# Optimization experiments

Hardware: AMD Instinct MI355X
Metric: run time of the kernel (lower is better)

## Reference

```python
import jax, jax.numpy as jnp
import numpy as np

B, N, E = 128, 100, 800          # graphs, nodes/graph, edges/graph
TN, TE = B * N, B * E
NODE_EMB, REL_EMB, H = 128, 256, 256   # hidden_size == relation_emb in CoMPILE
R, DEPTH = 200, 3
EDGE_EMB = 2 * NODE_EMB + REL_EMB      # 512


def _gru_dir(x, h0, w_ih, w_hh, b_ih, b_hh):
    """One direction of a torch-style GRU. x: [B,T,H], h0: [B,H] -> [B,T,H]."""
    def step(h, xt):
        gi = xt @ w_ih.T + b_ih
        gh = h @ w_hh.T + b_hh
        i_r, i_z, i_n = jnp.split(gi, 3, axis=-1)
        h_r, h_z, h_n = jnp.split(gh, 3, axis=-1)
        r = jax.nn.sigmoid(i_r + h_r)
        z = jax.nn.sigmoid(i_z + h_z)
        n = jnp.tanh(i_n + r * h_n)
        hn = (1.0 - z) * n + z * h
        return hn, hn
    _, ys = jax.lax.scan(step, h0, jnp.swapaxes(x, 0, 1))
    return jnp.swapaxes(ys, 0, 1)


def setup_inputs() -> dict:
    key = jax.random.key(0)
    ks = iter(jax.random.split(key, 40))
    def w(shape):
        return jax.random.normal(next(ks), shape, jnp.float32) * 0.05
    inp = {}
    inp["node_feat"] = jax.random.normal(next(ks), (TN, NODE_EMB), jnp.float32)
    inp["rel_emb"] = jax.random.normal(next(ks), (R, REL_EMB), jnp.float32)  # final_relation_embeddings
    # model weights (bias=False everywhere except W_o, linear1, gru)
    inp["W_i_node"] = w((H, NODE_EMB))
    inp["W_i_edge"] = w((H, EDGE_EMB))
    inp["Wa1"] = w((H, 2 * H))          # input_attention1
    inp["Wa2"] = w((1, H))              # input_attention2
    inp["W_h_atom"] = w((DEPTH - 1, H, H))
    inp["W_h_bond"] = w((DEPTH - 1, H, H))
    inp["Wd1"] = w((DEPTH - 1, H, H + REL_EMB))  # Attention1_d
    inp["Wd2"] = w((DEPTH - 1, 1, H))            # Attention2_d
    inp["W_comm"] = w((H, 3 * H))       # communicate_mlp
    inp["gru_bias"] = w((H,))
    inp["w_ih_f"] = w((3 * H, H)); inp["w_hh_f"] = w((3 * H, H))
    inp["b_ih_f"] = w((3 * H,));   inp["b_hh_f"] = w((3 * H,))
    inp["w_ih_b"] = w((3 * H, H)); inp["w_hh_b"] = w((3 * H, H))
    inp["b_ih_b"] = w((3 * H,));   inp["b_hh_b"] = w((3 * H,))
    inp["W_o"] = w((H, 2 * H)); inp["b_o"] = w((H,))
    inp["W_lin1"] = w((1, H)); inp["b_lin1"] = w((1,))
    # graph structure: edges stay inside their own subgraph (block-diagonal batching)
    off = (jnp.arange(B, dtype=jnp.int64)[:, None] * N)
    inp["edge_src"] = (jax.random.randint(next(ks), (B, E), 0, N) + off).reshape(-1)
    inp["edge_dst"] = (jax.random.randint(next(ks), (B, E), 0, N) + off).reshape(-1)
    inp["edge_rel"] = jax.random.randint(next(ks), (TE,), 0, R)
    inp["batch_rel"] = jax.random.randint(next(ks), (B,), 0, R)
    inp["src_node"] = jax.random.randint(next(ks), (B,), 0, N) + jnp.arange(B) * N
    inp["tgt_node"] = jax.random.randint(next(ks), (B,), 0, N) + jnp.arange(B) * N
    return inp


def reference(node_feat, rel_emb, W_i_node, W_i_edge, Wa1, Wa2, W_h_atom, W_h_bond,
              Wd1, Wd2, W_comm, gru_bias, w_ih_f, w_hh_f, b_ih_f, b_hh_f,
              w_ih_b, w_hh_b, b_ih_b, b_hh_b, W_o, b_o, W_lin1, b_lin1,
              edge_src, edge_dst, edge_rel, batch_rel, src_node, tgt_node):
    act = jax.nn.relu  # args.activation = 'ReLU'
    tgt_rel = rel_emb[batch_rel]                              # [B,H] per-query relation
    e_rel = rel_emb[edge_rel]                                 # [TE,H]
    edge_feat = jnp.concatenate([node_feat[edge_src], e_rel, node_feat[edge_dst]], 1)  # [TE,EDGE_EMB]
    input_node = act(node_feat @ W_i_node.T)                  # [TN,H]
    message_node = input_node
    input_edge = act(edge_feat @ W_i_edge.T)                  # [TE,H]
    message_edge = input_edge
    edge_tgt_rel = jnp.repeat(tgt_rel, E, axis=0)             # [TE,H] target relation per edge
    total_source = jnp.repeat(src_node, E)                    # [TE] query head node per edge
    total_target = jnp.repeat(tgt_node, E)
    # input edge attention vs translational query embedding
    g_edge = message_node[total_source] + edge_tgt_rel - message_node[total_target]
    att = jnp.tanh(jnp.concatenate([message_edge, g_edge], 1) @ Wa1.T)
    att = jax.nn.sigmoid(att @ Wa2.T)
    message_edge = message_edge * att
    for d in range(DEPTH - 1):
        # edge->node aggregation (MySpMM with target-side incidence e2n_sp)
        agg = jax.ops.segment_sum(message_edge, edge_dst, num_segments=TN)
        message_node = act((message_node + agg) @ W_h_atom[d].T)
        # node->edge (e2n_sp2^T: gather source-node states per edge)
        message_edge = act(input_edge + message_node[edge_src] @ W_h_bond[d].T)
        att = jnp.tanh(jnp.concatenate([message_edge, edge_tgt_rel], 1) @ Wd1[d].T)
        att = jax.nn.sigmoid(att @ Wd2[d].T)
        message_edge = message_edge * att
    agg = jax.ops.segment_sum(message_edge, edge_dst, num_segments=TN)
    agg2 = jnp.concatenate([agg, message_node, input_node], 1) @ W_comm.T  # [TN,H]
    # BatchGRU: uniform graph sizes -> pad/unpad is a reshape
    msg = act(agg2 + gru_bias).reshape(B, N, H)
    h0 = agg2.reshape(B, N, H).max(axis=1)                    # per-graph max of hidden
    out_f = _gru_dir(msg, h0, w_ih_f, w_hh_f, b_ih_f, b_hh_f)
    out_b = _gru_dir(msg[:, ::-1], h0, w_ih_b, w_hh_b, b_ih_b, b_hh_b)[:, ::-1]
    a_message = act(jnp.concatenate([out_f, out_b], -1).reshape(TN, 2 * H))
    atom_h = act(a_message @ W_o.T + b_o)                     # [TN,H]
    conv = jnp.tanh(atom_h[src_node] + tgt_rel - atom_h[tgt_node])  # [B,H]
    return conv @ W_lin1.T + b_lin1                           # [B,1]
```

## Files before the change

kernel.cpp:

```cpp
#include <hip/hip_runtime.h>
#include <cstddef>

#define Bg 128
#define Nn 100
#define Eg 800
#define TNODE 12800
#define TEDGE 102400
#define HD 256
#define NEMB 128
#define REMB 256

typedef short bf8 __attribute__((ext_vector_type(8)));
typedef short bf4 __attribute__((ext_vector_type(4)));
typedef float f4  __attribute__((ext_vector_type(4)));

__device__ __forceinline__ float relu_(float x){ return x > 0.f ? x : 0.f; }
__device__ __forceinline__ float sigm_(float x){ return 1.f/(1.f + __expf(-x)); }
__device__ __forceinline__ float4 ld4(const float* p){ return *(const float4*)p; }
__device__ __forceinline__ void st4(float* p, float4 v){ *(float4*)p = v; }
__device__ __forceinline__ float4 add4(float4 a, float4 b){
    return float4{a.x+b.x, a.y+b.y, a.z+b.z, a.w+b.w};
}
__device__ __forceinline__ float4 relu4(float4 a){
    return float4{relu_(a.x), relu_(a.y), relu_(a.z), relu_(a.w)};
}
__device__ __forceinline__ short f2bf(float f){
    unsigned u = __float_as_uint(f);
    u += 0x7fff + ((u >> 16) & 1);
    return (short)(u >> 16);
}
__device__ __forceinline__ float bf2f(short s){
    return __uint_as_float(((unsigned)(unsigned short)s) << 16);
}
__device__ __forceinline__ void split4(float4 v, bf4& h, bf4& l){
    h.x = f2bf(v.x); l.x = f2bf(v.x - bf2f(h.x));
    h.y = f2bf(v.y); l.y = f2bf(v.y - bf2f(h.y));
    h.z = f2bf(v.z); l.z = f2bf(v.z - bf2f(h.z));
    h.w = f2bf(v.w); l.w = f2bf(v.w - bf2f(h.w));
}
__device__ __forceinline__ f4 mfma_(bf8 a, bf8 b, f4 c){
    return __builtin_amdgcn_mfma_f32_16x16x32_bf16(a, b, c, 0, 0, 0);
}

enum { A_PLAIN=0, A_ADD=1, A_RELUB=2, A_CLAMP=3, A_CAT3=4, A_CAT2R=5 };
enum { E_STORE=0, E_RELU=1, E_BIAS=2, E_BIASRELU=3 };

template<int AM, int EM>
__global__ __launch_bounds__(256, 2)
void mgemm(const float* __restrict__ A0, const float* __restrict__ A1,
           const float* __restrict__ A2, const float* __restrict__ W,
           const float* __restrict__ bias, float* __restrict__ C,
           int M, int N, int K, int lda, int wld)
{
    __shared__ short Ah[128][40], Al[128][40], Bh[128][40], Bl[128][40];
    const int t  = threadIdx.x;
    const int kc = t & 7, lr = t >> 3;
    const int lane = t & 63, wv = t >> 6;
    const int wm = wv >> 1, wn = wv & 1;
    const int frow = lane & 15, fk = (lane >> 4) * 8;
    const int row0 = blockIdx.y * 128, col0 = blockIdx.x * 128;

    f4 acc[4][4] = {};

    for (int k0 = 0; k0 < K; k0 += 32) {
        const int gk = k0 + kc * 4;
        const int kk = kc * 4;
        #pragma unroll
        for (int ri = 0; ri < 4; ri++) {
            int row = lr + 32 * ri;
            int grow = row0 + row;
            float4 v;
            if (AM == A_PLAIN) {
                v = ld4(A0 + (size_t)grow * lda + gk);
            } else if (AM == A_ADD) {
                v = add4(ld4(A0 + (size_t)grow * lda + gk),
                         ld4(A1 + (size_t)grow * lda + gk));
            } else if (AM == A_RELUB) {
                v = relu4(add4(ld4(A0 + (size_t)grow * lda + gk), ld4(A1 + gk)));
            } else if (AM == A_CLAMP) {
                int cr = grow < M ? grow : M - 1;
                v = ld4(A0 + (size_t)cr * lda + gk);
            } else if (AM == A_CAT3) {
                if (gk < HD)        v = ld4(A0 + (size_t)grow * HD + gk);
                else if (gk < 2*HD) v = ld4(A1 + (size_t)grow * HD + gk - HD);
                else                v = ld4(A2 + (size_t)grow * HD + gk - 2*HD);
            } else {
                v = (gk < HD) ? relu4(ld4(A0 + (size_t)grow * HD + gk))
                              : relu4(ld4(A1 + (size_t)grow * HD + gk - HD));
            }
            bf4 h, l; split4(v, h, l);
            *(bf4*)&Ah[row][kk] = h;
            *(bf4*)&Al[row][kk] = l;
        }
        #pragma unroll
        for (int ri = 0; ri < 4; ri++) {
            int wr = lr + 32 * ri;
            float4 v = ld4(W + (size_t)(col0 + wr) * wld + gk);
            bf4 h, l; split4(v, h, l);
            *(bf4*)&Bh[wr][kk] = h;
            *(bf4*)&Bl[wr][kk] = l;
        }
        __syncthreads();
        bf8 ah[4], al[4], bh[4], bl[4];
        #pragma unroll
        for (int mi = 0; mi < 4; mi++) {
            ah[mi] = *(const bf8*)&Ah[wm*64 + mi*16 + frow][fk];
            al[mi] = *(const bf8*)&Al[wm*64 + mi*16 + frow][fk];
        }
        #pragma unroll
        for (int ni = 0; ni < 4; ni++) {
            bh[ni] = *(const bf8*)&Bh[wn*64 + ni*16 + frow][fk];
            bl[ni] = *(const bf8*)&Bl[wn*64 + ni*16 + frow][fk];
        }
        #pragma unroll
        for (int mi = 0; mi < 4; mi++)
            #pragma unroll
            for (int ni = 0; ni < 4; ni++) {
                acc[mi][ni] = mfma_(ah[mi], bh[ni], acc[mi][ni]);
                acc[mi][ni] = mfma_(ah[mi], bl[ni], acc[mi][ni]);
                acc[mi][ni] = mfma_(al[mi], bh[ni], acc[mi][ni]);
            }
        __syncthreads();
    }
    #pragma unroll
    for (int mi = 0; mi < 4; mi++) {
        #pragma unroll
        for (int ni = 0; ni < 4; ni++) {
            int ccol = col0 + wn*64 + ni*16 + frow;
            int rbase = row0 + wm*64 + mi*16 + (lane >> 4) * 4;
            #pragma unroll
            for (int reg = 0; reg < 4; reg++) {
                float v = acc[mi][ni][reg];
                if (EM == E_BIAS || EM == E_BIASRELU) v += bias[ccol];
                if (EM == E_RELU || EM == E_BIASRELU) v = relu_(v);
                C[(size_t)(rbase + reg) * N + ccol] = v;
            }
        }
    }
}

__global__ void w1split_kernel(const float* __restrict__ Wa1, const float* __restrict__ Wd1,
                               short* __restrict__ w1h, short* __restrict__ w1l)
{
    int idx = blockIdx.x * 256 + threadIdx.x;
    int which = idx >> 16, rem = idx & 65535;
    int r = rem >> 8, k = rem & 255;
    const float* W = (which == 0) ? Wa1 : (Wd1 + (size_t)(which - 1) * 256 * 512);
    float v = W[(size_t)r * 512 + k];
    short hi = f2bf(v);
    w1h[idx] = hi;
    w1l[idx] = f2bf(v - bf2f(hi));
}

template<int MODE>
__global__ __launch_bounds__(256, 2)
void mattn(const float* __restrict__ S, const float* __restrict__ Rt,
           const float* __restrict__ D, const float* __restrict__ T0,
           const int* __restrict__ esrc, const int* __restrict__ erel,
           const int* __restrict__ edst,
           const short* __restrict__ w1h, const short* __restrict__ w1l,
           const float* __restrict__ W2,
           const float* __restrict__ term, float* __restrict__ sbuf)
{
    __shared__ short Ah[128][40], Al[128][40];
    __shared__ float partl[4][128];
    __shared__ int isrc[128], irel[128], idst[128];
    const int t = threadIdx.x;
    const int kc = t & 7, lr = t >> 3;
    const int lane = t & 63, wv = t >> 6;
    const int frow = lane & 15, kb = (lane >> 4) * 8;
    const int r0 = blockIdx.x * 128;

    if (t < 128) {
        int e = r0 + t;
        isrc[t] = esrc[e]; irel[t] = erel[e]; idst[t] = edst[e];
    }
    __syncthreads();

    f4 acc[8][4] = {};

    for (int k0 = 0; k0 < 8; k0++) {
        const int gk = k0 * 32 + kc * 4;
        const int kk = kc * 4;
        #pragma unroll
        for (int ri = 0; ri < 4; ri++) {
            int row = lr + 32 * ri;
            int s = isrc[row], rl = irel[row], dd = idst[row];
            float4 v = relu4(add4(add4(ld4(S + (size_t)s * HD + gk),
                                       ld4(Rt + (size_t)rl * HD + gk)),
                                  ld4(D + (size_t)dd * HD + gk)));
            if (MODE) v = relu4(add4(v, ld4(T0 + (size_t)s * HD + gk)));
            bf4 h, l; split4(v, h, l);
            *(bf4*)&Ah[row][kk] = h;
            *(bf4*)&Al[row][kk] = l;
        }
        __syncthreads();
        bf8 ah[8], al[8];
        #pragma unroll
        for (int mi = 0; mi < 8; mi++) {
            ah[mi] = *(const bf8*)&Ah[mi*16 + frow][kb];
            al[mi] = *(const bf8*)&Al[mi*16 + frow][kb];
        }
        #pragma unroll
        for (int ni = 0; ni < 4; ni++) {
            int wr = wv*64 + ni*16 + frow;
            const short* wp = (const short*)w1h + (size_t)wr * 256 + k0*32 + kb;
            const short* lp = (const short*)w1l + (size_t)wr * 256 + k0*32 + kb;
            bf8 bh = *(const bf8*)wp;
            bf8 bl = *(const bf8*)lp;
            #pragma unroll
            for (int mi = 0; mi < 8; mi++) {
                acc[mi][ni] = mfma_(ah[mi], bh, acc[mi][ni]);
                acc[mi][ni] = mfma_(ah[mi], bl, acc[mi][ni]);
                acc[mi][ni] = mfma_(al[mi], bh, acc[mi][ni]);
            }
        }
        __syncthreads();
    }
    #pragma unroll
    for (int mi = 0; mi < 8; mi++) {
        #pragma unroll
        for (int reg = 0; reg < 4; reg++) {
            int rl = mi*16 + (lane >> 4) * 4 + reg;
            int g = (r0 + rl) / Eg;
            float p = 0.f;
            #pragma unroll
            for (int ni = 0; ni < 4; ni++) {
                int n = wv*64 + ni*16 + frow;
                p += tanhf(acc[mi][ni][reg] + term[g*HD + n]) * W2[n];
            }
            p += __shfl_xor(p, 1); p += __shfl_xor(p, 2);
            p += __shfl_xor(p, 4); p += __shfl_xor(p, 8);
            if (frow == 0) partl[wv][rl] = p;
        }
    }
    __syncthreads();
    if (t < 128) {
        float p = partl[0][t] + partl[1][t] + partl[2][t] + partl[3][t];
        sbuf[r0 + t] = sigm_(p);
    }
}

template<int MODE>
__global__ __launch_bounds__(256)
void agg_gather(const float* __restrict__ S, const float* __restrict__ Rt,
                const float* __restrict__ D, const float* __restrict__ T0,
                const int* __restrict__ esrc, const int* __restrict__ erel,
                const int* __restrict__ rowptr, const int* __restrict__ eidx,
                const float* __restrict__ s, float* __restrict__ agg)
{
    int node = blockIdx.x * 4 + (threadIdx.x >> 6);
    int c = (threadIdx.x & 63) * 4;
    float4 dn = ld4(D + (size_t)node * HD + c);
    float4 acc{0.f, 0.f, 0.f, 0.f};
    int beg = rowptr[node], end = rowptr[node + 1];
    for (int i = beg; i < end; i++) {
        int e = eidx[i];
        int sr = esrc[e], rl = erel[e];
        float4 v = relu4(add4(add4(ld4(S + (size_t)sr * HD + c),
                                   ld4(Rt + (size_t)rl * HD + c)), dn));
        if (MODE) v = relu4(add4(v, ld4(T0 + (size_t)sr * HD + c)));
        float sc = s[e];
        acc.x += v.x * sc; acc.y += v.y * sc;
        acc.z += v.z * sc; acc.w += v.w * sc;
    }
    st4(agg + (size_t)node * HD + c, acc);
}

__global__ void zeroi_kernel(int* __restrict__ p)
{
    p[blockIdx.x * 256 + threadIdx.x] = 0;
}
__global__ void csr_count(const int* __restrict__ dst, int* __restrict__ cnt)
{
    int e = blockIdx.x * 256 + threadIdx.x;
    atomicAdd(&cnt[dst[e]], 1);
}
__global__ void csr_scan(const int* __restrict__ cnt, int* __restrict__ rowptr)
{
    __shared__ int ws[4];
    __shared__ int carry;
    int tid = threadIdx.x;
    if (tid == 0) carry = 0;
    __syncthreads();
    for (int i = 0; i < TNODE; i += 256) {
        int v = cnt[i + tid];
        int x = v;
        #pragma unroll
        for (int off = 1; off < 64; off <<= 1) {
            int y = __shfl_up(x, off);
            if ((tid & 63) >= off) x += y;
        }
        if ((tid & 63) == 63) ws[tid >> 6] = x;
        __syncthreads();
        int add = carry;
        int w = tid >> 6;
        for (int j = 0; j < w; j++) add += ws[j];
        rowptr[i + tid] = add + x - v;
        __syncthreads();
        if (tid == 255) carry = add + x;
        __syncthreads();
    }
    if (tid == 0) rowptr[TNODE] = carry;
}
__global__ void csr_fill(const int* __restrict__ dst, const int* __restrict__ rowptr,
                         int* __restrict__ fillc, int* __restrict__ eidx)
{
    int e = blockIdx.x * 256 + threadIdx.x;
    int d = dst[e];
    int slot = rowptr[d] + atomicAdd(&fillc[d], 1);
    eidx[slot] = e;
}

__global__ __launch_bounds__(256)
void term_kernel(const float* __restrict__ mn, const float* __restrict__ tgt_rel,
                 const float* __restrict__ Wa1, const float* __restrict__ Wd1,
                 const int* __restrict__ srcn, const int* __restrict__ tgtn,
                 float* __restrict__ term)
{
    __shared__ float Gs[HD];
    int b = blockIdx.x % Bg;
    int which = blockIdx.x / Bg;
    int c = threadIdx.x;
    float g;
    if (which == 0)
        g = mn[(size_t)srcn[b]*HD + c] + tgt_rel[b*HD + c] - mn[(size_t)tgtn[b]*HD + c];
    else
        g = tgt_rel[b*HD + c];
    Gs[c] = g;
    __syncthreads();
    const float* W = (which == 0) ? Wa1 : (Wd1 + (size_t)(which-1)*HD*512);
    float p = 0.f;
    for (int k = 0; k < HD; k += 4) {
        float4 w = ld4(W + (size_t)c*512 + 256 + k);
        p = fmaf(Gs[k], w.x, p); p = fmaf(Gs[k+1], w.y, p);
        p = fmaf(Gs[k+2], w.z, p); p = fmaf(Gs[k+3], w.w, p);
    }
    term[(size_t)which*Bg*HD + b*HD + c] = p;
}

__global__ void tgtrel_kernel(const float* __restrict__ rel_emb, const int* __restrict__ batch_rel,
                              float* __restrict__ tgt_rel)
{
    int b = blockIdx.x, c = threadIdx.x;
    tgt_rel[b*HD + c] = rel_emb[(size_t)batch_rel[b]*REMB + c];
}

__global__ void h0_kernel(const float* __restrict__ agg2, float* __restrict__ h0)
{
    int b = blockIdx.x, c = threadIdx.x;
    float m = -1e30f;
    for (int n = 0; n < Nn; n++)
        m = fmaxf(m, agg2[((size_t)b*Nn + n)*HD + c]);
    h0[b*HD + c] = m;
}

__global__ void whbf_kernel(const float* __restrict__ whf, const float* __restrict__ whb,
                            short* __restrict__ whbf)
{
    int idx = blockIdx.x * 256 + threadIdx.x;
    int d = idx / (768*256), rem = idx % (768*256);
    whbf[idx] = f2bf((d ? whb : whf)[rem]);
}

__global__ void biascomb_kernel(const float* __restrict__ bihf, const float* __restrict__ bhhf,
                                const float* __restrict__ bihb, const float* __restrict__ bhhb,
                                float* __restrict__ bc)
{
    int i = blockIdx.x * 256 + threadIdx.x;
    int d = i / 768, r = i % 768;
    const float* bi = d ? bihb : bihf;
    const float* bhh = d ? bhhb : bhhf;
    bc[i] = bi[r] + (r < 512 ? bhh[r] : 0.f);
}

__global__ __launch_bounds__(512, 2)
void gru_seq(const float* __restrict__ gi_f, const float* __restrict__ gi_b,
             const short* __restrict__ whbf,
             const float* __restrict__ bhf, const float* __restrict__ bhb,
             const float* __restrict__ h0,
             float* __restrict__ outf, float* __restrict__ outb)
{
    __shared__ float hsf[16][260];
    __shared__ short hsh[16][264];
    __shared__ short hsl[16][264];
    __shared__ float gates[768][17];
    const int blk = blockIdx.x;
    const int d = blk >> 3, grp = blk & 7;
    const int tid = threadIdx.x;
    const int lane = tid & 63, wv = tid >> 6;
    const int f16 = lane & 15;
    const int kb  = (lane >> 4) * 8;

    const short* wp0 = whbf + (size_t)d * 768 * 256;
    const float* gi  = d ? gi_b : gi_f;
    const float* bh  = d ? bhb : bhf;
    float* outp      = d ? outb : outf;

    const int eseq = tid >> 5, ehb = tid & 31;
    float bhn[8];
    #pragma unroll
    for (int hh = 0; hh < 8; hh++) bhn[hh] = bh[512 + ehb + hh * 32];

    {
        #pragma unroll
        for (int hh = 0; hh < 8; hh++) {
            int h = ehb + hh * 32;
            float v = h0[(size_t)(grp*16 + eseq) * HD + h];
            hsf[eseq][h] = v;
            short hi = f2bf(v);
            hsh[eseq][h] = hi;
            hsl[eseq][h] = f2bf(v - bf2f(hi));
        }
    }
    __syncthreads();

    for (int t = 0; t < Nn; t++) {
        int trow = d ? (Nn - 1 - t) : t;
        float gr[8], gz[8], gn[8];
        {
            size_t girow = ((size_t)(grp*16 + eseq) * Nn + trow) * 768;
            #pragma unroll
            for (int hh = 0; hh < 8; hh++) {
                int h = ehb + hh * 32;
                gr[hh] = gi[girow + h];
                gz[hh] = gi[girow + 256 + h];
                gn[hh] = gi[girow + 512 + h];
            }
        }
        #pragma unroll
        for (int j = 0; j < 6; j++) {
            int wr = (wv*6 + j) * 16 + f16;
            const short* wp = wp0 + (size_t)wr * 256 + kb;
            f4 acc = {};
            #pragma unroll
            for (int ks = 0; ks < 8; ks++) {
                bf8 ahi = *(const bf8*)&hsh[f16][ks*32 + kb];
                bf8 alo = *(const bf8*)&hsl[f16][ks*32 + kb];
                bf8 b = *(const bf8*)(wp + ks*32);
                acc = mfma_(ahi, b, acc);
                acc = mfma_(alo, b, acc);
            }
            #pragma unroll
            for (int reg = 0; reg < 4; reg++)
                gates[(wv*6 + j)*16 + f16][(lane >> 4)*4 + reg] = acc[reg];
        }
        __syncthreads();
        {
            size_t orow = ((size_t)(grp*16 + eseq) * Nn + trow) * HD;
            #pragma unroll
            for (int hh = 0; hh < 8; hh++) {
                int h = ehb + hh * 32;
                float R  = gates[h][eseq];
                float Z  = gates[256 + h][eseq];
                float NN = gates[512 + h][eseq];
                float hprev = hsf[eseq][h];
                float r = sigm_(gr[hh] + R);
                float z = sigm_(gz[hh] + Z);
                float n = tanhf(gn[hh] + r * (NN + bhn[hh]));
                float nh = (1.f - z) * n + z * hprev;
                hsf[eseq][h] = nh;
                short hi = f2bf(nh);
                hsh[eseq][h] = hi;
                hsl[eseq][h] = f2bf(nh - bf2f(hi));
                outp[orow + h] = nh;
            }
        }
        __syncthreads();
    }
}

__global__ __launch_bounds__(256)
void final_kernel(const float* __restrict__ atom_h, const float* __restrict__ tgt_rel,
                  const int* __restrict__ srcn, const int* __restrict__ tgtn,
                  const float* __restrict__ Wl, const float* __restrict__ bl,
                  float* __restrict__ out)
{
    __shared__ float red[4];
    int b = blockIdx.x, c = threadIdx.x;
    float v = tanhf(atom_h[(size_t)srcn[b]*HD + c] + tgt_rel[b*HD + c]
                    - atom_h[(size_t)tgtn[b]*HD + c]);
    float p = v * Wl[c];
    #pragma unroll
    for (int off = 1; off < 64; off <<= 1) p += __shfl_xor(p, off);
    int wv = c >> 6;
    if ((c & 63) == 0) red[wv] = p;
    __syncthreads();
    if (c == 0) out[b] = red[0] + red[1] + red[2] + red[3] + bl[0];
}

extern "C" void kernel_launch(void* const* d_in, const int* in_sizes, int n_in,
                              void* d_out, int out_size, void* d_ws, size_t ws_size,
                              hipStream_t stream)
{
    const float* node_feat = (const float*)d_in[0];
    const float* rel_emb   = (const float*)d_in[1];
    const float* W_i_node  = (const float*)d_in[2];
    const float* W_i_edge  = (const float*)d_in[3];
    const float* Wa1       = (const float*)d_in[4];
    const float* Wa2       = (const float*)d_in[5];
    const float* W_h_atom  = (const float*)d_in[6];
    const float* W_h_bond  = (const float*)d_in[7];
    const float* Wd1       = (const float*)d_in[8];
    const float* Wd2       = (const float*)d_in[9];
    const float* W_comm    = (const float*)d_in[10];
    const float* gru_bias  = (const float*)d_in[11];
    const float* w_ih_f    = (const float*)d_in[12];
    const float* w_hh_f    = (const float*)d_in[13];
    const float* b_ih_f    = (const float*)d_in[14];
    const float* b_hh_f    = (const float*)d_in[15];
    const float* w_ih_b    = (const float*)d_in[16];
    const float* w_hh_b    = (const float*)d_in[17];
    const float* b_ih_b    = (const float*)d_in[18];
    const float* b_hh_b    = (const float*)d_in[19];
    const float* W_o       = (const float*)d_in[20];
    const float* b_o       = (const float*)d_in[21];
    const float* W_lin1    = (const float*)d_in[22];
    const float* b_lin1    = (const float*)d_in[23];
    const int* edge_src  = (const int*)d_in[24];
    const int* edge_dst  = (const int*)d_in[25];
    const int* edge_rel  = (const int*)d_in[26];
    const int* batch_rel = (const int*)d_in[27];
    const int* src_node  = (const int*)d_in[28];
    const int* tgt_node  = (const int*)d_in[29];
    float* out = (float*)d_out;

    float* ws = (float*)d_ws;
    size_t off = 0;
    auto alloc = [&](size_t n){ float* p = ws + off; off += n; return p; };
    float* tgt_rel    = alloc((size_t)Bg*HD);
    float* term       = alloc((size_t)3*Bg*HD);
    float* input_node = alloc((size_t)TNODE*HD);
    float* mn_a       = alloc((size_t)TNODE*HD);
    float* mn_b       = alloc((size_t)TNODE*HD);
    float* agg        = alloc((size_t)TNODE*HD);
    float* h0v        = alloc((size_t)Bg*HD);
    short* whbf       = (short*)alloc((size_t)2*768*256/2);
    short* w1h        = (short*)alloc((size_t)3*256*256/2);
    short* w1l        = (short*)alloc((size_t)3*256*256/2);
    float* bcomb      = alloc((size_t)2*768);
    float* sbuf       = alloc((size_t)TEDGE);
    int*   cnt        = (int*)alloc((size_t)TNODE);
    int*   fillc      = (int*)alloc((size_t)TNODE);
    int*   rowptr     = (int*)alloc((size_t)TNODE + 256);
    int*   eidx       = (int*)alloc((size_t)TEDGE);
    float* Sbuf       = alloc((size_t)TNODE*HD);
    float* Dbuf       = alloc((size_t)TNODE*HD);
    float* Rbuf       = alloc((size_t)256*HD);
    float* gi_f       = alloc((size_t)TNODE*768);
    float* gi_b       = alloc((size_t)TNODE*768);
    float* out_f      = alloc((size_t)TNODE*HD);
    float* out_b      = alloc((size_t)TNODE*HD);
    float* agg2   = mn_a;
    float* atom_h = input_node;

    tgtrel_kernel<<<Bg, 256, 0, stream>>>(rel_emb, batch_rel, tgt_rel);
    whbf_kernel<<<1536, 256, 0, stream>>>(w_hh_f, w_hh_b, whbf);
    w1split_kernel<<<768, 256, 0, stream>>>(Wa1, Wd1, w1h, w1l);
    biascomb_kernel<<<6, 256, 0, stream>>>(b_ih_f, b_hh_f, b_ih_b, b_hh_b, bcomb);

    zeroi_kernel<<<2*TNODE/256, 256, 0, stream>>>(cnt);
    csr_count<<<TEDGE/256, 256, 0, stream>>>(edge_dst, cnt);
    csr_scan<<<1, 256, 0, stream>>>(cnt, rowptr);
    csr_fill<<<TEDGE/256, 256, 0, stream>>>(edge_dst, rowptr, fillc, eidx);

    mgemm<A_PLAIN, E_RELU><<<dim3(HD/128, TNODE/128), 256, 0, stream>>>(
        node_feat, nullptr, nullptr, W_i_node, nullptr, input_node,
        TNODE, HD, NEMB, NEMB, NEMB);

    mgemm<A_PLAIN, E_STORE><<<dim3(HD/128, TNODE/128), 256, 0, stream>>>(
        node_feat, nullptr, nullptr, W_i_edge + 0, nullptr, Sbuf,
        TNODE, HD, NEMB, NEMB, 512);
    mgemm<A_PLAIN, E_STORE><<<dim3(HD/128, TNODE/128), 256, 0, stream>>>(
        node_feat, nullptr, nullptr, W_i_edge + 384, nullptr, Dbuf,
        TNODE, HD, NEMB, NEMB, 512);
    mgemm<A_CLAMP, E_STORE><<<dim3(HD/128, 2), 256, 0, stream>>>(
        rel_emb, nullptr, nullptr, W_i_edge + 128, nullptr, Rbuf,
        200, HD, REMB, REMB, 512);

    term_kernel<<<3*Bg, 256, 0, stream>>>(input_node, tgt_rel, Wa1, Wd1,
                                          src_node, tgt_node, term);

    mattn<0><<<TEDGE/128, 256, 0, stream>>>(Sbuf, Rbuf, Dbuf, Sbuf,
        edge_src, edge_rel, edge_dst, w1h, w1l, Wa2, term, sbuf);
    agg_gather<0><<<TNODE/4, 256, 0, stream>>>(Sbuf, Rbuf, Dbuf, Sbuf,
        edge_src, edge_rel, rowptr, eidx, sbuf, agg);

    const float* mn_cur = input_node;
    float* bufs[2] = {mn_a, mn_b};
    for (int d = 0; d < 2; d++) {
        float* mn_next = bufs[d];
        float* tmp     = bufs[1-d];
        mgemm<A_ADD, E_RELU><<<dim3(2, TNODE/128), 256, 0, stream>>>(
            mn_cur, agg, nullptr, W_h_atom + (size_t)d*HD*HD, nullptr, mn_next,
            TNODE, HD, HD, HD, HD);
        mgemm<A_PLAIN, E_STORE><<<dim3(2, TNODE/128), 256, 0, stream>>>(
            mn_next, nullptr, nullptr, W_h_bond + (size_t)d*HD*HD, nullptr, tmp,
            TNODE, HD, HD, HD, HD);
        mattn<1><<<TEDGE/128, 256, 0, stream>>>(Sbuf, Rbuf, Dbuf, tmp,
            edge_src, edge_rel, edge_dst, w1h + (size_t)(1+d)*65536,
            w1l + (size_t)(1+d)*65536, Wd2 + (size_t)d*HD,
            term + (size_t)(1+d)*Bg*HD, sbuf);
        agg_gather<1><<<TNODE/4, 256, 0, stream>>>(Sbuf, Rbuf, Dbuf, tmp,
            edge_src, edge_rel, rowptr, eidx, sbuf, agg);
        mn_cur = mn_next;
    }

    mgemm<A_CAT3, E_STORE><<<dim3(2, TNODE/128), 256, 0, stream>>>(
        agg, (const float*)mn_cur, input_node, W_comm, nullptr, agg2,
        TNODE, HD, 3*HD, 0, 3*HD);

    h0_kernel<<<Bg, 256, 0, stream>>>(agg2, h0v);

    mgemm<A_RELUB, E_BIAS><<<dim3(768/128, TNODE/128), 256, 0, stream>>>(
        agg2, gru_bias, nullptr, w_ih_f, bcomb, gi_f,
        TNODE, 768, HD, HD, HD);
    mgemm<A_RELUB, E_BIAS><<<dim3(768/128, TNODE/128), 256, 0, stream>>>(
        agg2, gru_bias, nullptr, w_ih_b, bcomb + 768, gi_b,
        TNODE, 768, HD, HD, HD);

    gru_seq<<<16, 512, 0, stream>>>(gi_f, gi_b, whbf, b_hh_f, b_hh_b, h0v,
                                    out_f, out_b);

    mgemm<A_CAT2R, E_BIASRELU><<<dim3(2, TNODE/128), 256, 0, stream>>>(
        out_f, out_b, nullptr, W_o, b_o, atom_h,
        TNODE, HD, 2*HD, 0, 2*HD);

    final_kernel<<<Bg, 256, 0, stream>>>(atom_h, tgt_rel, src_node, tgt_node,
                                         W_lin1, b_lin1, out);
}
```

Before: 1.319 ms.

## Pre-split GEMM weights into bf16 hi/lo once, read B fragments from global

Adds a generic wsplit kernel that converts each weight matrix into bf16 high/low halves once per call. The GEMM kernel then loads B fragments straight from global memory instead of staging and splitting weights in shared memory every tile. It also halves LDS use and raises launch bounds to three blocks per CU. The intent is to remove repeated per-block weight conversion and the LDS traffic for B. In exchange it adds twelve small split launches and uncoalesced global loads for B fragments, which depend on L2 hits.

```diff
diff --git a/kernel.cpp b/kernel.cpp
--- a/kernel.cpp
+++ b/kernel.cpp
@@ -45,14 +45,27 @@
 enum { A_PLAIN=0, A_ADD=1, A_RELUB=2, A_CLAMP=3, A_CAT3=4, A_CAT2R=5 };
 enum { E_STORE=0, E_RELU=1, E_BIAS=2, E_BIASRELU=3 };
 
+__global__ void wsplit(const float* __restrict__ src, int ld, int K,
+                       short* __restrict__ h, short* __restrict__ l, int total)
+{
+    int idx = blockIdx.x * 256 + threadIdx.x;
+    if (idx >= total) return;
+    int r = idx / K, k = idx % K;
+    float v = src[(size_t)r * ld + k];
+    short hi = f2bf(v);
+    h[idx] = hi;
+    l[idx] = f2bf(v - bf2f(hi));
+}
+
 template<int AM, int EM>
-__global__ __launch_bounds__(256, 2)
-void mgemm(const float* __restrict__ A0, const float* __restrict__ A1,
-           const float* __restrict__ A2, const float* __restrict__ W,
+__global__ __launch_bounds__(256, 3)
+void mgemw(const float* __restrict__ A0, const float* __restrict__ A1,
+           const float* __restrict__ A2,
+           const short* __restrict__ Wh, const short* __restrict__ Wl,
            const float* __restrict__ bias, float* __restrict__ C,
-           int M, int N, int K, int lda, int wld)
-{
-    __shared__ short Ah[128][40], Al[128][40], Bh[128][40], Bl[128][40];
+           int M, int N, int K, int lda)
+{
+    __shared__ short Ah[128][40], Al[128][40];
     const int t  = threadIdx.x;
     const int kc = t & 7, lr = t >> 3;
     const int lane = t & 63, wv = t >> 6;
@@ -92,14 +105,6 @@
             *(bf4*)&Ah[row][kk] = h;
             *(bf4*)&Al[row][kk] = l;
         }
-        #pragma unroll
-        for (int ri = 0; ri < 4; ri++) {
-            int wr = lr + 32 * ri;
-            float4 v = ld4(W + (size_t)(col0 + wr) * wld + gk);
-            bf4 h, l; split4(v, h, l);
-            *(bf4*)&Bh[wr][kk] = h;
-            *(bf4*)&Bl[wr][kk] = l;
-        }
         __syncthreads();
         bf8 ah[4], al[4], bh[4], bl[4];
         #pragma unroll
@@ -109,8 +114,9 @@
         }
         #pragma unroll
         for (int ni = 0; ni < 4; ni++) {
-            bh[ni] = *(const bf8*)&Bh[wn*64 + ni*16 + frow][fk];
-            bl[ni] = *(const bf8*)&Bl[wn*64 + ni*16 + frow][fk];
+            int wr = col0 + wn*64 + ni*16 + frow;
+            bh[ni] = *(const bf8*)&Wh[(size_t)wr * K + k0 + fk];
+            bl[ni] = *(const bf8*)&Wl[(size_t)wr * K + k0 + fk];
         }
         #pragma unroll
         for (int mi = 0; mi < 4; mi++)
@@ -137,19 +143,6 @@
             }
         }
     }
-}
-
-__global__ void w1split_kernel(const float* __restrict__ Wa1, const float* __restrict__ Wd1,
-                               short* __restrict__ w1h, short* __restrict__ w1l)
-{
-    int idx = blockIdx.x * 256 + threadIdx.x;
-    int which = idx >> 16, rem = idx & 65535;
-    int r = rem >> 8, k = rem & 255;
-    const float* W = (which == 0) ? Wa1 : (Wd1 + (size_t)(which - 1) * 256 * 512);
-    float v = W[(size_t)r * 512 + k];
-    short hi = f2bf(v);
-    w1h[idx] = hi;
-    w1l[idx] = f2bf(v - bf2f(hi));
 }
 
 template<int MODE>
@@ -204,10 +197,8 @@
         #pragma unroll
         for (int ni = 0; ni < 4; ni++) {
             int wr = wv*64 + ni*16 + frow;
-            const short* wp = (const short*)w1h + (size_t)wr * 256 + k0*32 + kb;
-            const short* lp = (const short*)w1l + (size_t)wr * 256 + k0*32 + kb;
-            bf8 bh = *(const bf8*)wp;
-            bf8 bl = *(const bf8*)lp;
+            bf8 bh = *(const bf8*)(w1h + (size_t)wr * 256 + k0*32 + kb);
+            bf8 bl = *(const bf8*)(w1l + (size_t)wr * 256 + k0*32 + kb);
             #pragma unroll
             for (int mi = 0; mi < 8; mi++) {
                 acc[mi][ni] = mfma_(ah[mi], bh, acc[mi][ni]);
@@ -528,6 +519,7 @@
     float* ws = (float*)d_ws;
     size_t off = 0;
     auto alloc = [&](size_t n){ float* p = ws + off; off += n; return p; };
+    auto salloc = [&](size_t n){ short* p = (short*)(ws + off); off += (n + 1) / 2; return p; };
     float* tgt_rel    = alloc((size_t)Bg*HD);
     float* term       = alloc((size_t)3*Bg*HD);
     float* input_node = alloc((size_t)TNODE*HD);
@@ -535,9 +527,18 @@
     float* mn_b       = alloc((size_t)TNODE*HD);
     float* agg        = alloc((size_t)TNODE*HD);
     float* h0v        = alloc((size_t)Bg*HD);
-    short* whbf       = (short*)alloc((size_t)2*768*256/2);
-    short* w1h        = (short*)alloc((size_t)3*256*256/2);
-    short* w1l        = (short*)alloc((size_t)3*256*256/2);
+    short* whbf       = salloc((size_t)2*768*256);
+    short* w1h        = salloc((size_t)3*256*256);
+    short* w1l        = salloc((size_t)3*256*256);
+    short* wnh  = salloc(256*128);  short* wnl  = salloc(256*128);
+    short* wsh  = salloc(256*128);  short* wsl  = salloc(256*128);
+    short* wrh  = salloc(256*256);  short* wrl  = salloc(256*256);
+    short* wdh  = salloc(256*128);  short* wdl  = salloc(256*128);
+    short* whah = salloc(2*256*256); short* whal = salloc(2*256*256);
+    short* whbh = salloc(2*256*256); short* whbl = salloc(2*256*256);
+    short* wch  = salloc(256*768);  short* wcl  = salloc(256*768);
+    short* wihh = salloc(2*768*256); short* wihl = salloc(2*768*256);
+    short* woh  = salloc(256*512);  short* wol  = salloc(256*512);
     float* bcomb      = alloc((size_t)2*768);
     float* sbuf       = alloc((size_t)TEDGE);
     int*   cnt        = (int*)alloc((size_t)TNODE);
@@ -556,27 +557,42 @@
 
     tgtrel_kernel<<<Bg, 256, 0, stream>>>(rel_emb, batch_rel, tgt_rel);
     whbf_kernel<<<1536, 256, 0, stream>>>(w_hh_f, w_hh_b, whbf);
-    w1split_kernel<<<768, 256, 0, stream>>>(Wa1, Wd1, w1h, w1l);
     biascomb_kernel<<<6, 256, 0, stream>>>(b_ih_f, b_hh_f, b_ih_b, b_hh_b, bcomb);
+
+    {
+        __global__ void (*noop)() = nullptr; (void)noop;
+    }
+    wsplit<<<768, 256, 0, stream>>>(Wa1, 512, 256, w1h, w1l, 65536);
+    wsplit<<<768, 256, 0, stream>>>(Wd1, 512, 256, w1h + 65536, w1l + 65536, 131072);
+    wsplit<<<128, 256, 0, stream>>>(W_i_node, 128, 128, wnh, wnl, 32768);
+    wsplit<<<128, 256, 0, stream>>>(W_i_edge + 0, 512, 128, wsh, wsl, 32768);
+    wsplit<<<256, 256, 0, stream>>>(W_i_edge + 128, 512, 256, wrh, wrl, 65536);
+    wsplit<<<128, 256, 0, stream>>>(W_i_edge + 384, 512, 128, wdh, wdl, 32768);
+    wsplit<<<512, 256, 0, stream>>>(W_h_atom, 256, 256, whah, whal, 131072);
+    wsplit<<<512, 256, 0, stream>>>(W_h_bond, 256, 256, whbh, whbl, 131072);
+    wsplit<<<768, 256, 0, stream>>>(W_comm, 768, 768, wch, wcl, 196608);
+    wsplit<<<768, 256, 0, stream>>>(w_ih_f, 256, 256, wihh, wihl, 196608);
+    wsplit<<<768, 256, 0, stream>>>(w_ih_b, 256, 256, wihh + 196608, wihl + 196608, 196608);
+    wsplit<<<512, 256, 0, stream>>>(W_o, 512, 512, woh, wol, 131072);
 
     zeroi_kernel<<<2*TNODE/256, 256, 0, stream>>>(cnt);
     csr_count<<<TEDGE/256, 256, 0, stream>>>(edge_dst, cnt);
     csr_scan<<<1, 256, 0, stream>>>(cnt, rowptr);
     csr_fill<<<TEDGE/256, 256, 0, stream>>>(edge_dst, rowptr, fillc, eidx);
 
-    mgemm<A_PLAIN, E_RELU><<<dim3(HD/128, TNODE/128), 256, 0, stream>>>(
-        node_feat, nullptr, nullptr, W_i_node, nullptr, input_node,
-        TNODE, HD, NEMB, NEMB, NEMB);
-
-    mgemm<A_PLAIN, E_STORE><<<dim3(HD/128, TNODE/128), 256, 0, stream>>>(
-        node_feat, nullptr, nullptr, W_i_edge + 0, nullptr, Sbuf,
-        TNODE, HD, NEMB, NEMB, 512);
-    mgemm<A_PLAIN, E_STORE><<<dim3(HD/128, TNODE/128), 256, 0, stream>>>(
-        node_feat, nullptr, nullptr, W_i_edge + 384, nullptr, Dbuf,
-        TNODE, HD, NEMB, NEMB, 512);
-    mgemm<A_CLAMP, E_STORE><<<dim3(HD/128, 2), 256, 0, stream>>>(
-        rel_emb, nullptr, nullptr, W_i_edge + 128, nullptr, Rbuf,
-        200, HD, REMB, REMB, 512);
+    mgemw<A_PLAIN, E_RELU><<<dim3(HD/128, TNODE/128), 256, 0, stream>>>(
+        node_feat, nullptr, nullptr, wnh, wnl, nullptr, input_node,
+        TNODE, HD, NEMB, NEMB);
+
+    mgemw<A_PLAIN, E_STORE><<<dim3(HD/128, TNODE/128), 256, 0, stream>>>(
+        node_feat, nullptr, nullptr, wsh, wsl, nullptr, Sbuf,
+        TNODE, HD, NEMB, NEMB);
+    mgemw<A_PLAIN, E_STORE><<<dim3(HD/128, TNODE/128), 256, 0, stream>>>(
+        node_feat, nullptr, nullptr, wdh, wdl, nullptr, Dbuf,
+        TNODE, HD, NEMB, NEMB);
+    mgemw<A_CLAMP, E_STORE><<<dim3(HD/128, 2), 256, 0, stream>>>(
+        rel_emb, nullptr, nullptr, wrh, wrl, nullptr, Rbuf,
+        200, HD, REMB, REMB);
 
     term_kernel<<<3*Bg, 256, 0, stream>>>(input_node, tgt_rel, Wa1, Wd1,
                                           src_node, tgt_node, term);
@@ -591,12 +607,12 @@
     for (int d = 0; d < 2; d++) {
         float* mn_next = bufs[d];
         float* tmp     = bufs[1-d];
-        mgemm<A_ADD, E_RELU><<<dim3(2, TNODE/128), 256, 0, stream>>>(
-            mn_cur, agg, nullptr, W_h_atom + (size_t)d*HD*HD, nullptr, mn_next,
-            TNODE, HD, HD, HD, HD);
-        mgemm<A_PLAIN, E_STORE><<<dim3(2, TNODE/128), 256, 0, stream>>>(
-            mn_next, nullptr, nullptr, W_h_bond + (size_t)d*HD*HD, nullptr, tmp,
-            TNODE, HD, HD, HD, HD);
+        mgemw<A_ADD, E_RELU><<<dim3(2, TNODE/128), 256, 0, stream>>>(
+            mn_cur, agg, nullptr, whah + (size_t)d*65536, whal + (size_t)d*65536,
+            nullptr, mn_next, TNODE, HD, HD, HD);
+        mgemw<A_PLAIN, E_STORE><<<dim3(2, TNODE/128), 256, 0, stream>>>(
+            mn_next, nullptr, nullptr, whbh + (size_t)d*65536, whbl + (size_t)d*65536,
+            nullptr, tmp, TNODE, HD, HD, HD);
         mattn<1><<<TEDGE/128, 256, 0, stream>>>(Sbuf, Rbuf, Dbuf, tmp,
             edge_src, edge_rel, edge_dst, w1h + (size_t)(1+d)*65536,
             w1l + (size_t)(1+d)*65536, Wd2 + (size_t)d*HD,
@@ -606,25 +622,25 @@
         mn_cur = mn_next;
     }
 
-    mgemm<A_CAT3, E_STORE><<<dim3(2, TNODE/128), 256, 0, stream>>>(
-        agg, (const float*)mn_cur, input_node, W_comm, nullptr, agg2,
-        TNODE, HD, 3*HD, 0, 3*HD);
+    mgemw<A_CAT3, E_STORE><<<dim3(2, TNODE/128), 256, 0, stream>>>(
+        agg, (const float*)mn_cur, input_node, wch, wcl, nullptr, agg2,
+        TNODE, HD, 3*HD, 0);
 
     h0_kernel<<<Bg, 256, 0, stream>>>(agg2, h0v);
 
-    mgemm<A_RELUB, E_BIAS><<<dim3(768/128, TNODE/128), 256, 0, stream>>>(
-        agg2, gru_bias, nullptr, w_ih_f, bcomb, gi_f,
-        TNODE, 768, HD, HD, HD);
-    mgemm<A_RELUB, E_BIAS><<<dim3(768/128, TNODE/128), 256, 0, stream>>>(
-        agg2, gru_bias, nullptr, w_ih_b, bcomb + 768, gi_b,
-        TNODE, 768, HD, HD, HD);
+    mgemw<A_RELUB, E_BIAS><<<dim3(768/128, TNODE/128), 256, 0, stream>>>(
+        agg2, gru_bias, nullptr, wihh, wihl, bcomb, gi_f,
+        TNODE, 768, HD, HD);
+    mgemw<A_RELUB, E_BIAS><<<dim3(768/128, TNODE/128), 256, 0, stream>>>(
+        agg2, gru_bias, nullptr, wihh + 196608, wihl + 196608, bcomb + 768, gi_b,
+        TNODE, 768, HD, HD);
 
     gru_seq<<<16, 512, 0, stream>>>(gi_f, gi_b, whbf, b_hh_f, b_hh_b, h0v,
                                     out_f, out_b);
 
-    mgemm<A_CAT2R, E_BIASRELU><<<dim3(2, TNODE/128), 256, 0, stream>>>(
-        out_f, out_b, nullptr, W_o, b_o, atom_h,
-        TNODE, HD, 2*HD, 0, 2*HD);
+    mgemw<A_CAT2R, E_BIASRELU><<<dim3(2, TNODE/128), 256, 0, stream>>>(
+        out_f, out_b, nullptr, woh, wol, b_o, atom_h,
+        TNODE, HD, 2*HD, 0);
 
     final_kernel<<<Bg, 256, 0, stream>>>(atom_h, tgt_rel, src_node, tgt_node,
                                          W_lin1, b_lin1, out);
```

After: 1.346 ms. 2.0% more time.
